# Optimization experiments

Hardware: AMD Instinct MI355X
Metric: run time of the kernel (lower is better)

Reference implementation:

```python
import jax, jax.numpy as jnp
import numpy as np
import math

HIDDEN = 1024
INTER = 4096
HEADS = 16
HEAD_DIM = 64
INNER = HEADS * HEAD_DIM
SEQ = 4096


def setup_inputs() -> dict:
    key = jax.random.key(0)
    ks = jax.random.split(key, 16)
    s = 0.02
    d = dict(
        x=jax.random.normal(ks[0], (SEQ, HIDDEN), dtype=jnp.float32),
        # attention norm
        an_w=jnp.ones((HIDDEN,), jnp.float32),
        an_b=jnp.zeros((HIDDEN,), jnp.float32),
        # attention projections (weight stored as [out, in] like torch)
        q_w=jax.random.normal(ks[1], (INNER, HIDDEN)) * s,
        q_b=jnp.zeros((INNER,), jnp.float32),
        k_w=jax.random.normal(ks[2], (INNER, HIDDEN)) * s,
        k_b=jnp.zeros((INNER,), jnp.float32),
        v_w=jax.random.normal(ks[3], (INNER, HIDDEN)) * s,
        v_b=jnp.zeros((INNER,), jnp.float32),
        o_w=jax.random.normal(ks[4], (HIDDEN, INNER)) * s,
        o_b=jnp.zeros((HIDDEN,), jnp.float32),
        # ff norm
        fn_w=jnp.ones((HIDDEN,), jnp.float32),
        fn_b=jnp.zeros((HIDDEN,), jnp.float32),
        ff1_w=jax.random.normal(ks[5], (INTER, HIDDEN)) * s,
        ff1_b=jnp.zeros((INTER,), jnp.float32),
        ff2_w=jax.random.normal(ks[6], (HIDDEN, INTER)) * s,
        ff2_b=jnp.zeros((HIDDEN,), jnp.float32),
    )
    return d


def _norm_novar(x, w, b):
    # mean-only layer norm (no variance normalization)
    return w * (x - jnp.mean(x, axis=-1, keepdims=True)) + b


def _block(x, an_w, an_b, q_w, q_b, k_w, k_b, v_w, v_b, o_w, o_b,
           fn_w, fn_b, ff1_w, ff1_b, ff2_w, ff2_b):
    S = x.shape[0]
    scale = math.sqrt(HEAD_DIM)
    xn = _norm_novar(x, an_w, an_b)
    # [S, inner] -> [h, S, d]
    Q = (xn @ q_w.T + q_b).reshape(S, HEADS, HEAD_DIM).transpose(1, 0, 2)
    K = (xn @ k_w.T + k_b).reshape(S, HEADS, HEAD_DIM).transpose(1, 0, 2)
    V = (xn @ v_w.T + v_b).reshape(S, HEADS, HEAD_DIM).transpose(1, 0, 2)
    scores = jnp.einsum('hsd,htd->hst', Q, K) / scale  # [h, S, S]
    attn = jax.nn.softmax(scores, axis=-1)
    ctx = jnp.einsum('hst,htd->hsd', attn, V)  # [h, S, d]
    ctx = ctx.transpose(1, 0, 2).reshape(S, INNER)
    x = ctx @ o_w.T + o_b + x
    xn = _norm_novar(x, fn_w, fn_b)
    h = jax.nn.relu(xn @ ff1_w.T + ff1_b)
    return h @ ff2_w.T + ff2_b + x


def reference(x, an_w, an_b, q_w, q_b, k_w, k_b, v_w, v_b, o_w, o_b,
              fn_w, fn_b, ff1_w, ff1_b, ff2_w, ff2_b):
    return _block(x, an_w, an_b, q_w, q_b, k_w, k_b, v_w, v_b, o_w, o_b,
                  fn_w, fn_b, ff1_w, ff1_b, ff2_w, ff2_b)
```

## Files before the change

kernel.cpp:

```cpp
#include <hip/hip_runtime.h>
#include <hip/hip_bf16.h>

#define SQ 4096
#define HID 1024
#define INTER_DIM 4096
#define NH 16
#define DH 64
#define SCALE_Q 0.18033688f

typedef __attribute__((ext_vector_type(4))) float f32x4;
typedef __attribute__((ext_vector_type(16))) float f32x16;
typedef __attribute__((ext_vector_type(8))) short bf16x8;

__device__ __forceinline__ unsigned short f2bf(float f) {
  union { float f; unsigned int i; } v; v.f = f;
  unsigned int i = v.i;
  return (unsigned short)((i + 0x7FFFu + ((i >> 16) & 1u)) >> 16);
}

__device__ __forceinline__ void load_lds16(const void* g, void* l) {
  __builtin_amdgcn_global_load_lds(
      (const __attribute__((address_space(1))) void*)g,
      (__attribute__((address_space(3))) void*)l, 16, 0, 0);
}

__device__ __forceinline__ int cvtpk_bf16(float a, float b) {
  int r;
  asm("v_cvt_pk_bf16_f32 %0, %1, %2" : "=v"(r) : "v"(a), "v"(b));
  return r;
}

__device__ __forceinline__ float fexp2(float x) {
  float r;
  asm("v_exp_f32 %0, %1\n\ts_nop 1" : "=v"(r) : "v"(x));
  return r;
}

__global__ __launch_bounds__(256) void cvt6_kernel(
    const float* __restrict__ s0, const float* __restrict__ s1,
    const float* __restrict__ s2, const float* __restrict__ s3,
    const float* __restrict__ s4, const float* __restrict__ s5,
    unsigned short* __restrict__ dst) {
  const int b = blockIdx.x;
  const float* src;
  int lb;
  size_t base4;
  if (b < 4096) {
    const int r = b >> 10;
    lb = b & 1023;
    src = (r == 0) ? s0 : (r == 1) ? s1 : (r == 2) ? s2 : s3;
    base4 = (size_t)r << 18;
  } else if (b < 8192) {
    lb = b - 4096; src = s4; base4 = 1u << 20;
  } else {
    lb = b - 8192; src = s5; base4 = 2u << 20;
  }
  const float sc = (b < 1024) ? SCALE_Q : 1.0f;
  const int i = lb * 256 + threadIdx.x;
  const float4 v4 = ((const float4*)src)[i];
  ushort4 o4;
  o4.x = f2bf(v4.x * sc); o4.y = f2bf(v4.y * sc);
  o4.z = f2bf(v4.z * sc); o4.w = f2bf(v4.w * sc);
  ((ushort4*)dst)[base4 + i] = o4;
}

__global__ __launch_bounds__(256) void bias3_kernel(
    const float* __restrict__ qb, const float* __restrict__ kb,
    const float* __restrict__ vb, float* __restrict__ dst) {
  const int b = blockIdx.x, t = threadIdx.x;
  const float* s = (b == 0) ? qb : (b == 1) ? kb : vb;
  float4 v = ((const float4*)s)[t];
  if (b == 0) { v.x *= SCALE_Q; v.y *= SCALE_Q; v.z *= SCALE_Q; v.w *= SCALE_Q; }
  ((float4*)dst)[b * 256 + t] = v;
}

__global__ __launch_bounds__(256) void ln_kernel(
    const float* __restrict__ x, const float* __restrict__ w,
    const float* __restrict__ b, unsigned short* __restrict__ out) {
  const int row = blockIdx.x;
  const int t = threadIdx.x;
  const float4 v = ((const float4*)(x + (size_t)row * HID))[t];
  float s = v.x + v.y + v.z + v.w;
  #pragma unroll
  for (int off = 32; off > 0; off >>= 1) s += __shfl_xor(s, off);
  __shared__ float red[4];
  if ((t & 63) == 0) red[t >> 6] = s;
  __syncthreads();
  const float mean = (red[0] + red[1] + red[2] + red[3]) * (1.0f / HID);
  const float4 wv = ((const float4*)w)[t];
  const float4 bv = ((const float4*)b)[t];
  ushort4 o;
  o.x = f2bf(wv.x * (v.x - mean) + bv.x);
  o.y = f2bf(wv.y * (v.y - mean) + bv.y);
  o.z = f2bf(wv.z * (v.z - mean) + bv.z);
  o.w = f2bf(wv.w * (v.w - mean) + bv.w);
  ((ushort4*)(out + (size_t)row * HID))[t] = o;
}

__global__ __launch_bounds__(256) void combine_kernel(
    float* __restrict__ out, const float* __restrict__ p1,
    const float* __restrict__ res) {
  const int i = blockIdx.x * 256 + threadIdx.x;
  float4 o = ((const float4*)out)[i];
  const float4 a = ((const float4*)p1)[i];
  const float4 r = ((const float4*)res)[i];
  o.x += a.x + r.x; o.y += a.y + r.y; o.z += a.z + r.z; o.w += a.w + r.w;
  ((float4*)out)[i] = o;
}

template <int MODE>
__global__ __launch_bounds__(256) void gemm_bt(
    const unsigned short* __restrict__ A, const unsigned short* __restrict__ B,
    const float* __restrict__ bias, const float* __restrict__ res,
    void* __restrict__ Cout, void* __restrict__ Cout2, int M, int N, int K) {
  __shared__ __align__(16) unsigned short As[2][128 * 32];
  __shared__ __align__(16) unsigned short Bs[2][128 * 32];
  const int t = threadIdx.x;
  const int lane = t & 63;
  const int wave = t >> 6;
  const int g = lane >> 4;
  const int lr = lane & 15;
  const int waveM = wave >> 1, waveN = wave & 1;
  const int rowBase = blockIdx.x * 128;
  const int colBase = blockIdx.y * 128;
  const int Keff = (MODE == 5) ? (K >> 1) : K;
  const int kBase = (MODE == 5) ? blockIdx.z * Keff : 0;

  f32x4 acc[4][4];
  #pragma unroll
  for (int m = 0; m < 4; ++m)
    #pragma unroll
    for (int n = 0; n < 4; ++n) acc[m][n] = (f32x4){0.f, 0.f, 0.f, 0.f};

  const int c0 = t, c1 = t + 256;
  const int r0s = c0 >> 2, s0 = (c0 & 3) ^ (r0s & 3);
  const int r1s = c1 >> 2, s1 = (c1 & 3) ^ (r1s & 3);
  const unsigned short* gA0 = A + (size_t)(rowBase + r0s) * K + kBase + s0 * 8;
  const unsigned short* gA1 = A + (size_t)(rowBase + r1s) * K + kBase + s1 * 8;
  const unsigned short* gB0 = B + (size_t)(colBase + r0s) * K + kBase + s0 * 8;
  const unsigned short* gB1 = B + (size_t)(colBase + r1s) * K + kBase + s1 * 8;

  load_lds16(gA0, &As[0][wave * 512]);
  load_lds16(gA1, &As[0][2048 + wave * 512]);
  load_lds16(gB0, &Bs[0][wave * 512]);
  load_lds16(gB1, &Bs[0][2048 + wave * 512]);
  __syncthreads();

  const int nk = Keff >> 5;
  for (int kt = 0; kt < nk; ++kt) {
    const int buf = kt & 1;
    if (kt + 1 < nk) {
      const int k0 = (kt + 1) << 5;
      load_lds16(gA0 + k0, &As[buf ^ 1][wave * 512]);
      load_lds16(gA1 + k0, &As[buf ^ 1][2048 + wave * 512]);
      load_lds16(gB0 + k0, &Bs[buf ^ 1][wave * 512]);
      load_lds16(gB1 + k0, &Bs[buf ^ 1][2048 + wave * 512]);
    }
    bf16x8 af[4], bfr[4];
    #pragma unroll
    for (int m = 0; m < 4; ++m) {
      const int r = waveM * 64 + m * 16 + lr;
      af[m] = *(const bf16x8*)&As[buf][r * 32 + ((g ^ (r & 3)) << 3)];
    }
    #pragma unroll
    for (int n = 0; n < 4; ++n) {
      const int c = waveN * 64 + n * 16 + lr;
      bfr[n] = *(const bf16x8*)&Bs[buf][c * 32 + ((g ^ (c & 3)) << 3)];
    }
    #pragma unroll
    for (int m = 0; m < 4; ++m)
      #pragma unroll
      for (int n = 0; n < 4; ++n)
        acc[m][n] = __builtin_amdgcn_mfma_f32_16x16x32_bf16(af[m], bfr[n],
                                                            acc[m][n], 0, 0, 0);
    __syncthreads();
  }

  const int crow0 = rowBase + waveM * 64;
  const int ccol0 = colBase + waveN * 64;
  #pragma unroll
  for (int n = 0; n < 4; ++n) {
    const int col = ccol0 + n * 16 + lr;
    const float bv = bias[col];
    #pragma unroll
    for (int m = 0; m < 4; ++m) {
      const int row0 = crow0 + m * 16 + g * 4;
      if (MODE == 4) {
        if (col < 2048) {
          #pragma unroll
          for (int j = 0; j < 4; ++j)
            ((unsigned short*)Cout)[(size_t)(row0 + j) * 2048 + col] =
                f2bf(acc[m][n][j] + bv);
        } else {
          ushort4 o4;
          o4.x = f2bf(acc[m][n][0] + bv);
          o4.y = f2bf(acc[m][n][1] + bv);
          o4.z = f2bf(acc[m][n][2] + bv);
          o4.w = f2bf(acc[m][n][3] + bv);
          *(ushort4*)&((unsigned short*)Cout2)[(size_t)(col - 2048) * M + row0] = o4;
        }
      } else if (MODE == 1) {
        #pragma unroll
        for (int j = 0; j < 4; ++j)
          ((unsigned short*)Cout)[(size_t)(row0 + j) * N + col] =
              f2bf(fmaxf(acc[m][n][j] + bv, 0.f));
      } else if (MODE == 5) {
        if (blockIdx.z == 0) {
          #pragma unroll
          for (int j = 0; j < 4; ++j)
            ((float*)Cout)[(size_t)(row0 + j) * N + col] = acc[m][n][j] + bv;
        } else {
          #pragma unroll
          for (int j = 0; j < 4; ++j)
            ((float*)Cout2)[(size_t)(row0 + j) * N + col] = acc[m][n][j];
        }
      } else {
        #pragma unroll
        for (int j = 0; j < 4; ++j)
          ((float*)Cout)[(size_t)(row0 + j) * N + col] =
              acc[m][n][j] + bv + res[(size_t)(row0 + j) * N + col];
      }
    }
  }
}

__global__ __launch_bounds__(256, 2) void attn_kernel(
    const unsigned short* __restrict__ QK,
    const unsigned short* __restrict__ Vt,
    unsigned short* __restrict__ ctx) {
  const int s = blockIdx.y * gridDim.x + blockIdx.x;
  const int q6 = s >> 3;
  const int h = (s & 7) * 2 + (q6 >> 5);
  const int qt = q6 & 31;

  const int t = threadIdx.x;
  const int lane = t & 63;
  const int wave = t >> 6;
  const int ql = lane & 31;
  const int hi = lane >> 5;

  __shared__ __align__(16) unsigned short Ks[2][64 * 64];
  __shared__ __align__(16) unsigned short Vs[2][64 * 64];

  const int qbase = qt * 128 + wave * 32;
  const unsigned short* qptr =
      QK + (size_t)(qbase + ql) * 2048 + h * DH + hi * 8;
  bf16x8 qf[4];
  #pragma unroll
  for (int ks = 0; ks < 4; ++ks) qf[ks] = *(const bf16x8*)(qptr + ks * 16);

  const int cr = t >> 3, cs = t & 7;
  const int cr2 = cr + 32;
  const unsigned short* gK0 =
      QK + (size_t)cr * 2048 + 1024 + h * DH + ((cs ^ (cr & 7)) << 3);
  const unsigned short* gK1 =
      QK + (size_t)cr2 * 2048 + 1024 + h * DH + ((cs ^ (cr2 & 7)) << 3);
  const unsigned short* gV0 = Vt + (size_t)(h * DH + cr) * SQ + ((cs ^ (cr & 7)) << 3);
  const unsigned short* gV1 = Vt + (size_t)(h * DH + cr2) * SQ + ((cs ^ (cr2 & 7)) << 3);

  float mreg = 0.f, lreg = 0.f;
  f32x16 oacc0 = 0.f, oacc1 = 0.f;

  load_lds16(gK0, &Ks[0][wave * 512]);
  load_lds16(gK1, &Ks[0][2048 + wave * 512]);
  load_lds16(gV0, &Vs[0][wave * 512]);
  load_lds16(gV1, &Vs[0][2048 + wave * 512]);

  for (int kt = 0; kt < SQ / 64; ++kt) {
    const int buf = kt & 1;
    __syncthreads();
    if (kt + 1 < SQ / 64) {
      const size_t ko = (size_t)(kt + 1) * 64 * 2048;
      const int vo = (kt + 1) * 64;
      load_lds16(gK0 + ko, &Ks[buf ^ 1][wave * 512]);
      load_lds16(gK1 + ko, &Ks[buf ^ 1][2048 + wave * 512]);
      load_lds16(gV0 + vo, &Vs[buf ^ 1][wave * 512]);
      load_lds16(gV1 + vo, &Vs[buf ^ 1][2048 + wave * 512]);
    }
    const unsigned short* KsB = &Ks[buf][0];
    const unsigned short* VsB = &Vs[buf][0];

    f32x16 st0, st1;
    #pragma unroll
    for (int r = 0; r < 16; ++r) { st0[r] = -mreg; st1[r] = -mreg; }
    __builtin_amdgcn_s_setprio(1);
    #pragma unroll
    for (int ks = 0; ks < 4; ++ks) {
      const int sl = ((((ks << 1) | hi) ^ (ql & 7)) << 3);
      const bf16x8 k0 = *(const bf16x8*)&KsB[ql * 64 + sl];
      const bf16x8 k1 = *(const bf16x8*)&KsB[(32 + ql) * 64 + sl];
      st0 = __builtin_amdgcn_mfma_f32_32x32x16_bf16(k0, qf[ks], st0, 0, 0, 0);
      st1 = __builtin_amdgcn_mfma_f32_32x32x16_bf16(k1, qf[ks], st1, 0, 0, 0);
    }
    __builtin_amdgcn_s_setprio(0);

    bf16x8 vf0[4], vf1[4];
    #pragma unroll
    for (int ks = 0; ks < 4; ++ks) {
      const int sl = ((((ks << 1) | hi) ^ (ql & 7)) << 3);
      vf0[ks] = *(const bf16x8*)&VsB[ql * 64 + sl];
      vf1[ks] = *(const bf16x8*)&VsB[(32 + ql) * 64 + sl];
    }

    float tr[16];
    #pragma unroll
    for (int r = 0; r < 16; ++r) tr[r] = fmaxf(st0[r], st1[r]);
    #pragma unroll
    for (int s2 = 8; s2 > 0; s2 >>= 1)
      #pragma unroll
      for (int r = 0; r < s2; ++r) tr[r] = fmaxf(tr[r], tr[r + s2]);
    const float mx = fmaxf(tr[0], __shfl_xor(tr[0], 32));

    if (!__all(mx <= 8.0f)) {
      const float mpos = fmaxf(mx, 0.f);
      const float corr = fexp2(-mpos);
      mreg += mpos;
      lreg *= corr;
      #pragma unroll
      for (int r = 0; r < 16; ++r) { st0[r] -= mpos; st1[r] -= mpos; }
      #pragma unroll
      for (int r = 0; r < 16; ++r) {
        const float c = __shfl(corr, (r & 3) + 8 * (r >> 2) + 4 * hi);
        oacc0[r] *= c;
        oacc1[r] *= c;
      }
    }

    #pragma unroll
    for (int r = 0; r < 16; ++r) st0[r] = fexp2(st0[r]);
    #pragma unroll
    for (int r = 0; r < 16; ++r) st1[r] = fexp2(st1[r]);
    float ts[16];
    #pragma unroll
    for (int r = 0; r < 16; ++r) ts[r] = st0[r] + st1[r];
    #pragma unroll
    for (int s2 = 8; s2 > 0; s2 >>= 1)
      #pragma unroll
      for (int r = 0; r < s2; ++r) ts[r] += ts[r + s2];
    lreg += ts[0] + __shfl_xor(ts[0], 32);

    union { int w[4]; bf16x8 v; } pa[4];
    #pragma unroll
    for (int half = 0; half < 2; ++half) {
      #pragma unroll
      for (int kk = 0; kk < 2; ++kk) {
        const int base = kk * 8;
        float p0, p1, p2, p3, p4, p5, p6, p7;
        if (half == 0) {
          p0 = st0[base + 0]; p1 = st0[base + 1]; p2 = st0[base + 2]; p3 = st0[base + 3];
          p4 = st0[base + 4]; p5 = st0[base + 5]; p6 = st0[base + 6]; p7 = st0[base + 7];
        } else {
          p0 = st1[base + 0]; p1 = st1[base + 1]; p2 = st1[base + 2]; p3 = st1[base + 3];
          p4 = st1[base + 4]; p5 = st1[base + 5]; p6 = st1[base + 6]; p7 = st1[base + 7];
        }
        const int d0 = cvtpk_bf16(p0, p1), sw0 = cvtpk_bf16(p4, p5);
        const int d1 = cvtpk_bf16(p2, p3), sw1 = cvtpk_bf16(p6, p7);
        auto a = __builtin_amdgcn_permlane32_swap(d0, sw0, false, false);
        auto b = __builtin_amdgcn_permlane32_swap(d1, sw1, false, false);
        const int ks = half * 2 + kk;
        pa[ks].w[0] = a[0]; pa[ks].w[1] = b[0];
        pa[ks].w[2] = a[1]; pa[ks].w[3] = b[1];
      }
    }

    __builtin_amdgcn_s_setprio(1);
    #pragma unroll
    for (int ks = 0; ks < 4; ++ks) {
      oacc0 = __builtin_amdgcn_mfma_f32_32x32x16_bf16(pa[ks].v, vf0[ks], oacc0, 0, 0, 0);
      oacc1 = __builtin_amdgcn_mfma_f32_32x32x16_bf16(pa[ks].v, vf1[ks], oacc1, 0, 0, 0);
    }
    __builtin_amdgcn_s_setprio(0);
  }

  const float linv = 1.0f / lreg;
  #pragma unroll
  for (int r = 0; r < 16; ++r) {
    const int qq = (r & 3) + 8 * (r >> 2) + 4 * hi;
    const float li = __shfl(linv, qq);
    unsigned short* cp = ctx + (size_t)(qbase + qq) * HID + h * DH + ql;
    cp[0] = f2bf(oacc0[r] * li);
    cp[32] = f2bf(oacc1[r] * li);
  }
}

extern "C" void kernel_launch(void* const* d_in, const int* in_sizes, int n_in,
                              void* d_out, int out_size, void* d_ws,
                              size_t ws_size, hipStream_t stream) {
  const float* x     = (const float*)d_in[0];
  const float* an_w  = (const float*)d_in[1];
  const float* an_b  = (const float*)d_in[2];
  const float* q_w   = (const float*)d_in[3];
  const float* q_b   = (const float*)d_in[4];
  const float* k_w   = (const float*)d_in[5];
  const float* k_b   = (const float*)d_in[6];
  const float* v_w   = (const float*)d_in[7];
  const float* v_b   = (const float*)d_in[8];
  const float* o_w   = (const float*)d_in[9];
  const float* o_b   = (const float*)d_in[10];
  const float* fn_w  = (const float*)d_in[11];
  const float* fn_b  = (const float*)d_in[12];
  const float* ff1_w = (const float*)d_in[13];
  const float* ff1_b = (const float*)d_in[14];
  const float* ff2_w = (const float*)d_in[15];
  const float* ff2_b = (const float*)d_in[16];

  char* ws = (char*)d_ws;
  const size_t MB = 1ull << 20;
  unsigned short* xn    = (unsigned short*)(ws + 0);
  unsigned short* qkvwb = (unsigned short*)(ws + 8 * MB);
  unsigned short* owb   = (unsigned short*)(ws + 14 * MB);
  unsigned short* f1wb  = (unsigned short*)(ws + 16 * MB);
  unsigned short* f2wb  = (unsigned short*)(ws + 24 * MB);
  unsigned short* QKm   = (unsigned short*)(ws + 32 * MB);
  unsigned short* Vtm   = (unsigned short*)(ws + 48 * MB);
  unsigned short* ctx   = (unsigned short*)(ws + 56 * MB);
  float*          bAll  = (float*)(ws + 56 * MB);
  float*          x2    = (float*)(ws + 64 * MB);
  unsigned short* hbuf  = (unsigned short*)(ws + 32 * MB);
  unsigned short* x2n   = xn;
  float*          p1    = (float*)(ws + 0);

  cvt6_kernel<<<12288, 256, 0, stream>>>(q_w, k_w, v_w, o_w, ff1_w, ff2_w, qkvwb);
  bias3_kernel<<<3, 256, 0, stream>>>(q_b, k_b, v_b, bAll);

  ln_kernel<<<SQ, 256, 0, stream>>>(x, an_w, an_b, xn);

  gemm_bt<4><<<dim3(SQ / 128, 3072 / 128), 256, 0, stream>>>(
      xn, qkvwb, bAll, nullptr, QKm, Vtm, SQ, 3072, HID);

  attn_kernel<<<dim3(32, 16), 256, 0, stream>>>(QKm, Vtm, ctx);

  gemm_bt<2><<<dim3(SQ / 128, HID / 128), 256, 0, stream>>>(
      ctx, owb, o_b, x, x2, nullptr, SQ, HID, HID);

  ln_kernel<<<SQ, 256, 0, stream>>>(x2, fn_w, fn_b, x2n);

  gemm_bt<1><<<dim3(SQ / 128, INTER_DIM / 128), 256, 0, stream>>>(
      x2n, f1wb, ff1_b, nullptr, hbuf, nullptr, SQ, INTER_DIM, HID);

  gemm_bt<5><<<dim3(SQ / 128, HID / 128, 2), 256, 0, stream>>>(
      hbuf, f2wb, ff2_b, nullptr, (float*)d_out, p1, SQ, HID, INTER_DIM);

  combine_kernel<<<(SQ * HID) / 1024, 256, 0, stream>>>((float*)d_out, p1, x2);
}
```

Measured before the change: 409.0 us.

## Halve attention block size and split-K the output projection

Attention blocks now use 2 waves covering 64 queries instead of 4 waves covering 128, which doubles the grid to 1024 blocks and shrinks per-block work. The K/V tile loads are redistributed across the smaller thread count. The output projection GEMM is split along K into two halves. One half writes fp32 with bias and the other writes bf16 partials, and a new combine kernel adds them together with the residual. This aims for more parallelism and better occupancy, but the K/V traffic per query is doubled, there is an extra launch, and the bf16 partial loses some precision.

After: 425.3 us. 4.0% more time.

```diff
diff --git a/kernel.cpp b/kernel.cpp
--- a/kernel.cpp
+++ b/kernel.cpp
@@ -12,6 +12,9 @@
 typedef __attribute__((ext_vector_type(16))) float f32x16;
 typedef __attribute__((ext_vector_type(8))) short bf16x8;
 
+__device__ __forceinline__ float bf2f(unsigned short u) {
+  union { float f; unsigned int i; } v; v.i = ((unsigned int)u) << 16; return v.f;
+}
 __device__ __forceinline__ unsigned short f2bf(float f) {
   union { float f; unsigned int i; } v; v.f = f;
   unsigned int i = v.i;
@@ -108,11 +111,23 @@
   ((float4*)out)[i] = o;
 }
 
+__global__ __launch_bounds__(256) void combineO_kernel(
+    float* __restrict__ x2, const unsigned short* __restrict__ p1,
+    const float* __restrict__ res) {
+  const int i = blockIdx.x * 256 + threadIdx.x;
+  float4 o = ((const float4*)x2)[i];
+  const ushort4 a = ((const ushort4*)p1)[i];
+  const float4 r = ((const float4*)res)[i];
+  o.x += bf2f(a.x) + r.x; o.y += bf2f(a.y) + r.y;
+  o.z += bf2f(a.z) + r.z; o.w += bf2f(a.w) + r.w;
+  ((float4*)x2)[i] = o;
+}
+
 template <int MODE>
 __global__ __launch_bounds__(256) void gemm_bt(
     const unsigned short* __restrict__ A, const unsigned short* __restrict__ B,
-    const float* __restrict__ bias, const float* __restrict__ res,
-    void* __restrict__ Cout, void* __restrict__ Cout2, int M, int N, int K) {
+    const float* __restrict__ bias, void* __restrict__ Cout,
+    void* __restrict__ Cout2, int M, int N, int K) {
   __shared__ __align__(16) unsigned short As[2][128 * 32];
   __shared__ __align__(16) unsigned short Bs[2][128 * 32];
   const int t = threadIdx.x;
@@ -123,8 +138,8 @@
   const int waveM = wave >> 1, waveN = wave & 1;
   const int rowBase = blockIdx.x * 128;
   const int colBase = blockIdx.y * 128;
-  const int Keff = (MODE == 5) ? (K >> 1) : K;
-  const int kBase = (MODE == 5) ? blockIdx.z * Keff : 0;
+  const int Keff = (MODE == 5 || MODE == 7) ? (K >> 1) : K;
+  const int kBase = (MODE == 5 || MODE == 7) ? blockIdx.z * Keff : 0;
 
   f32x4 acc[4][4];
   #pragma unroll
@@ -215,34 +230,40 @@
             ((float*)Cout2)[(size_t)(row0 + j) * N + col] = acc[m][n][j];
         }
       } else {
-        #pragma unroll
-        for (int j = 0; j < 4; ++j)
-          ((float*)Cout)[(size_t)(row0 + j) * N + col] =
-              acc[m][n][j] + bv + res[(size_t)(row0 + j) * N + col];
+        if (blockIdx.z == 0) {
+          #pragma unroll
+          for (int j = 0; j < 4; ++j)
+            ((float*)Cout)[(size_t)(row0 + j) * N + col] = acc[m][n][j] + bv;
+        } else {
+          #pragma unroll
+          for (int j = 0; j < 4; ++j)
+            ((unsigned short*)Cout2)[(size_t)(row0 + j) * N + col] =
+                f2bf(acc[m][n][j]);
+        }
       }
     }
   }
 }
 
-__global__ __launch_bounds__(256, 2) void attn_kernel(
+__global__ __launch_bounds__(128, 2) void attn_kernel(
     const unsigned short* __restrict__ QK,
     const unsigned short* __restrict__ Vt,
     unsigned short* __restrict__ ctx) {
   const int s = blockIdx.y * gridDim.x + blockIdx.x;
   const int q6 = s >> 3;
-  const int h = (s & 7) * 2 + (q6 >> 5);
-  const int qt = q6 & 31;
+  const int h = (s & 7) * 2 + (q6 >> 6);
+  const int qt = q6 & 63;
 
   const int t = threadIdx.x;
   const int lane = t & 63;
-  const int wave = t >> 6;
+  const int w = t >> 6;
   const int ql = lane & 31;
   const int hi = lane >> 5;
 
   __shared__ __align__(16) unsigned short Ks[2][64 * 64];
   __shared__ __align__(16) unsigned short Vs[2][64 * 64];
 
-  const int qbase = qt * 128 + wave * 32;
+  const int qbase = qt * 64 + w * 32;
   const unsigned short* qptr =
       QK + (size_t)(qbase + ql) * 2048 + h * DH + hi * 8;
   bf16x8 qf[4];
@@ -250,21 +271,18 @@
   for (int ks = 0; ks < 4; ++ks) qf[ks] = *(const bf16x8*)(qptr + ks * 16);
 
   const int cr = t >> 3, cs = t & 7;
-  const int cr2 = cr + 32;
-  const unsigned short* gK0 =
-      QK + (size_t)cr * 2048 + 1024 + h * DH + ((cs ^ (cr & 7)) << 3);
-  const unsigned short* gK1 =
-      QK + (size_t)cr2 * 2048 + 1024 + h * DH + ((cs ^ (cr2 & 7)) << 3);
-  const unsigned short* gV0 = Vt + (size_t)(h * DH + cr) * SQ + ((cs ^ (cr & 7)) << 3);
-  const unsigned short* gV1 = Vt + (size_t)(h * DH + cr2) * SQ + ((cs ^ (cr2 & 7)) << 3);
+  const int sw = (cs ^ (cr & 7)) << 3;
+  const unsigned short* gK0 = QK + (size_t)cr * 2048 + 1024 + h * DH + sw;
+  const unsigned short* gV0 = Vt + (size_t)(h * DH + cr) * SQ + sw;
 
   float mreg = 0.f, lreg = 0.f;
   f32x16 oacc0 = 0.f, oacc1 = 0.f;
 
-  load_lds16(gK0, &Ks[0][wave * 512]);
-  load_lds16(gK1, &Ks[0][2048 + wave * 512]);
-  load_lds16(gV0, &Vs[0][wave * 512]);
-  load_lds16(gV1, &Vs[0][2048 + wave * 512]);
+  #pragma unroll
+  for (int i = 0; i < 4; ++i) {
+    load_lds16(gK0 + (size_t)i * 16 * 2048, &Ks[0][i * 1024 + w * 512]);
+    load_lds16(gV0 + (size_t)i * 16 * SQ, &Vs[0][i * 1024 + w * 512]);
+  }
 
   for (int kt = 0; kt < SQ / 64; ++kt) {
     const int buf = kt & 1;
@@ -272,10 +290,13 @@
     if (kt + 1 < SQ / 64) {
       const size_t ko = (size_t)(kt + 1) * 64 * 2048;
       const int vo = (kt + 1) * 64;
-      load_lds16(gK0 + ko, &Ks[buf ^ 1][wave * 512]);
-      load_lds16(gK1 + ko, &Ks[buf ^ 1][2048 + wave * 512]);
-      load_lds16(gV0 + vo, &Vs[buf ^ 1][wave * 512]);
-      load_lds16(gV1 + vo, &Vs[buf ^ 1][2048 + wave * 512]);
+      #pragma unroll
+      for (int i = 0; i < 4; ++i) {
+        load_lds16(gK0 + ko + (size_t)i * 16 * 2048,
+                   &Ks[buf ^ 1][i * 1024 + w * 512]);
+        load_lds16(gV0 + vo + (size_t)i * 16 * SQ,
+                   &Vs[buf ^ 1][i * 1024 + w * 512]);
+      }
     }
     const unsigned short* KsB = &Ks[buf][0];
     const unsigned short* VsB = &Vs[buf][0];
@@ -339,7 +360,7 @@
       for (int r = 0; r < s2; ++r) ts[r] += ts[r + s2];
     lreg += ts[0] + __shfl_xor(ts[0], 32);
 
-    union { int w[4]; bf16x8 v; } pa[4];
+    union { int wd[4]; bf16x8 v; } pa[4];
     #pragma unroll
     for (int half = 0; half < 2; ++half) {
       #pragma unroll
@@ -358,8 +379,8 @@
         auto a = __builtin_amdgcn_permlane32_swap(d0, sw0, false, false);
         auto b = __builtin_amdgcn_permlane32_swap(d1, sw1, false, false);
         const int ks = half * 2 + kk;
-        pa[ks].w[0] = a[0]; pa[ks].w[1] = b[0];
-        pa[ks].w[2] = a[1]; pa[ks].w[3] = b[1];
+        pa[ks].wd[0] = a[0]; pa[ks].wd[1] = b[0];
+        pa[ks].wd[2] = a[1]; pa[ks].wd[3] = b[1];
       }
     }
 
@@ -407,6 +428,7 @@
   char* ws = (char*)d_ws;
   const size_t MB = 1ull << 20;
   unsigned short* xn    = (unsigned short*)(ws + 0);
+  unsigned short* p1o   = (unsigned short*)(ws + 0);
   unsigned short* qkvwb = (unsigned short*)(ws + 8 * MB);
   unsigned short* owb   = (unsigned short*)(ws + 14 * MB);
   unsigned short* f1wb  = (unsigned short*)(ws + 16 * MB);
@@ -426,20 +448,22 @@
   ln_kernel<<<SQ, 256, 0, stream>>>(x, an_w, an_b, xn);
 
   gemm_bt<4><<<dim3(SQ / 128, 3072 / 128), 256, 0, stream>>>(
-      xn, qkvwb, bAll, nullptr, QKm, Vtm, SQ, 3072, HID);
-
-  attn_kernel<<<dim3(32, 16), 256, 0, stream>>>(QKm, Vtm, ctx);
-
-  gemm_bt<2><<<dim3(SQ / 128, HID / 128), 256, 0, stream>>>(
-      ctx, owb, o_b, x, x2, nullptr, SQ, HID, HID);
+      xn, qkvwb, bAll, QKm, Vtm, SQ, 3072, HID);
+
+  attn_kernel<<<dim3(32, 32), 128, 0, stream>>>(QKm, Vtm, ctx);
+
+  gemm_bt<7><<<dim3(SQ / 128, HID / 128, 2), 256, 0, stream>>>(
+      ctx, owb, o_b, x2, p1o, SQ, HID, HID);
+  combineO_kernel<<<(SQ * HID / 4) / 256, 256, 0, stream>>>(x2, p1o, x);
 
   ln_kernel<<<SQ, 256, 0, stream>>>(x2, fn_w, fn_b, x2n);
 
   gemm_bt<1><<<dim3(SQ / 128, INTER_DIM / 128), 256, 0, stream>>>(
-      x2n, f1wb, ff1_b, nullptr, hbuf, nullptr, SQ, INTER_DIM, HID);
+      x2n, f1wb, ff1_b, hbuf, nullptr, SQ, INTER_DIM, HID);
 
   gemm_bt<5><<<dim3(SQ / 128, HID / 128, 2), 256, 0, stream>>>(
-      hbuf, f2wb, ff2_b, nullptr, (float*)d_out, p1, SQ, HID, INTER_DIM);
-
-  combine_kernel<<<(SQ * HID) / 1024, 256, 0, stream>>>((float*)d_out, p1, x2);
-}
+      hbuf, f2wb, ff2_b, (float*)d_out, p1, SQ, HID, INTER_DIM);
+
+  combine_kernel<<<(SQ * HID / 4) / 256, 256, 0, stream>>>(
+      (float*)d_out, p1, x2);
+}
```
